# Optimization experiments

Hardware: AMD Instinct MI355X
Metric: run time of the kernel (lower is better)

The kernel has to match this reference:

```python
import jax, jax.numpy as jnp
import numpy as np

BS, T, N, M, P = 1024, 128, 128, 256, 256


def _lstm_cell(xin, h, c, Wih, Whh, bih, bhh):
    # PyTorch LSTMCell: gates ordered i, f, g, o
    z = xin @ Wih.T + bih + h @ Whh.T + bhh
    i, f, g, o = jnp.split(z, 4, axis=1)
    i = jax.nn.sigmoid(i); f = jax.nn.sigmoid(f)
    g = jnp.tanh(g); o = jax.nn.sigmoid(o)
    c2 = f * c + i * g
    return o * jnp.tanh(c2), c2


def setup_inputs() -> dict:
    key = jax.random.key(0)
    ks = jax.random.split(key, 24)
    s = 0.05
    return {
        "x": jax.random.normal(ks[0], (BS, T, N), jnp.float32),
        "y_known": jax.random.normal(ks[1], (BS, T, 1), jnp.float32),
        "We": jax.random.normal(ks[2], (T, 2 * M), jnp.float32) * s,
        "Ue": jax.random.normal(ks[3], (T, T), jnp.float32) * s,
        "Ve": jax.random.normal(ks[4], (1, T), jnp.float32) * s,
        "Wih_e": jax.random.normal(ks[5], (4 * M, N), jnp.float32) * s,
        "Whh_e": jax.random.normal(ks[6], (4 * M, M), jnp.float32) * s,
        "bih_e": jax.random.normal(ks[7], (4 * M,), jnp.float32) * s,
        "bhh_e": jax.random.normal(ks[8], (4 * M,), jnp.float32) * s,
        "Wd": jax.random.normal(ks[9], (M, 2 * P), jnp.float32) * s,
        "Ud": jax.random.normal(ks[10], (M, M), jnp.float32) * s,
        "Vd": jax.random.normal(ks[11], (1, M), jnp.float32) * s,
        "Wih_d": jax.random.normal(ks[12], (4 * P, 1), jnp.float32) * s,
        "Whh_d": jax.random.normal(ks[13], (4 * P, P), jnp.float32) * s,
        "bih_d": jax.random.normal(ks[14], (4 * P,), jnp.float32) * s,
        "bhh_d": jax.random.normal(ks[15], (4 * P,), jnp.float32) * s,
        "Wt": jax.random.normal(ks[16], (1, M + 1), jnp.float32) * s,
        "bt": jax.random.normal(ks[17], (1,), jnp.float32) * s,
        "W1": jax.random.normal(ks[18], (P, P + M), jnp.float32) * s,
        "b1": jax.random.normal(ks[19], (P,), jnp.float32) * s,
        "W2": jax.random.normal(ks[20], (1, P), jnp.float32) * s,
        "b2": jax.random.normal(ks[21], (1,), jnp.float32) * s,
    }


def reference(x, y_known, We, Ue, Ve, Wih_e, Whh_e, bih_e, bhh_e,
              Wd, Ud, Vd, Wih_d, Whh_d, bih_d, bhh_d,
              Wt, bt, W1, b1, W2, b2):
    bs, Tl, n = x.shape
    m = Whh_e.shape[1]
    p = Whh_d.shape[1]

    # ---- encoder (input attention) ----
    # U_e(x.permute(0,2,1)): loop-invariant, hoisted. (bs, n, T)
    Ux = jnp.einsum('btn,st->bns', x, Ue)

    def enc_step(carry, _):
        h, s = carry
        hs = jnp.concatenate([h, s], axis=1)            # (bs, 2m)
        ohs = hs @ We.T                                  # (bs, T)
        tanh_sum = jnp.tanh(ohs[:, None, :] + Ux)        # (bs, n, T)
        e = jnp.einsum('bnt,t->bn', tanh_sum, Ve[0])     # (bs, n)
        alpha = jax.nn.softmax(e, axis=1)
        xt = alpha * e                                   # faithful quirk: alpha * e_t
        h2, s2 = _lstm_cell(xt, h, s, Wih_e, Whh_e, bih_e, bhh_e)
        return (h2, s2), h2

    z = jnp.zeros((bs, m), x.dtype)
    _, h_all = jax.lax.scan(enc_step, (z, z), None, length=Tl)
    x1 = jnp.transpose(h_all, (1, 2, 0))                 # (bs, m, T)

    # ---- decoder (temporal attention) ----
    Udx = jnp.einsum('bmt,km->btk', x1, Ud)              # (bs, T, m)

    def dec_step(carry, yt):
        d, s, _ = carry
        ds = jnp.concatenate([d, s], axis=1)             # (bs, 2p)
        ods = ds @ Wd.T                                   # (bs, m)
        tanh_sum = jnp.tanh(ods[:, None, :] + Udx)        # (bs, T, m)
        l = jnp.einsum('btm,m->bt', tanh_sum, Vd[0])      # (bs, T)
        beta = jax.nn.softmax(l, axis=1)
        c = jnp.einsum('bt,bmt->bm', beta, x1)            # (bs, m)
        y_tilde = jnp.concatenate([yt, c], axis=1) @ Wt.T + bt  # (bs, 1)
        d2, s2 = _lstm_cell(y_tilde, d, s, Wih_d, Whh_d, bih_d, bhh_d)
        return (d2, s2, c), None

    zp = jnp.zeros((bs, p), x.dtype)
    zc = jnp.zeros((bs, m), x.dtype)
    (d, _, c), _ = jax.lax.scan(dec_step, (zp, zp, zc),
                                jnp.transpose(y_known, (1, 0, 2)))
    out1 = jnp.concatenate([d, c], axis=1) @ W1.T + b1
    return out1 @ W2.T + b2
```

## Files before the change

kernel.cpp:

```cpp
#include <hip/hip_runtime.h>


typedef unsigned int   uint;
typedef unsigned short ushort;
typedef _Float16 h2v __attribute__((ext_vector_type(2)));

#define O_WEH     0u
#define O_WENCH   32768u
#define O_WDH     229376u
#define O_WHHDH   294912u
#define O_UDT     425984u
#define O_UET     491520u
#define O_W1T     507904u
#define O_BENC    638976u
#define O_BDEC    640000u
#define W_FLOATS  641024u
#define O_X1H     641024u
#define O_BUF     17418240u
#define WS_FLOATS 34195456u

#define C2E 2.8853900817779268f
#define L2E 1.4426950408889634f

#define FMA4(acc, s, w) \
  acc.x = fmaf((s), (w).x, acc.x); \
  acc.y = fmaf((s), (w).y, acc.y); \
  acc.z = fmaf((s), (w).z, acc.z); \
  acc.w = fmaf((s), (w).w, acc.w);

union H2U { uint u; h2v h; _Float16 hs[2]; };

__device__ __forceinline__ float fdot2u(uint w, uint s, float acc) {
  H2U a; a.u = w; H2U b; b.u = s;
  return __builtin_amdgcn_fdot2(a.h, b.h, acc, false);
}
__device__ __forceinline__ uint pk2(float lo, float hi) {
  H2U v; v.hs[0] = (_Float16)lo; v.hs[1] = (_Float16)hi; return v.u;
}
__device__ __forceinline__ float h2lo(uint u) { H2U v; v.u = u; return (float)v.hs[0]; }
__device__ __forceinline__ float h2hi(uint u) { H2U v; v.u = u; return (float)v.hs[1]; }

__device__ __forceinline__ float fsig(float x) {
  return __builtin_amdgcn_rcpf(1.f + __builtin_amdgcn_exp2f(-L2E * x));
}
__device__ __forceinline__ float fth(float x) {
  float r = __builtin_amdgcn_rcpf(1.f + __builtin_amdgcn_exp2f(C2E * x));
  return fmaf(-2.f, r, 1.f);
}

#define DOT8(w, s0, s1) { \
  a0 = fdot2u(w.x, s0, a0); a1 = fdot2u(w.y, s0, a1); \
  a2 = fdot2u(w.z, s0, a2); a3 = fdot2u(w.w, s0, a3); \
  b0 = fdot2u(w.x, s1, b0); b1 = fdot2u(w.y, s1, b1); \
  b2 = fdot2u(w.z, s1, b2); b3 = fdot2u(w.w, s1, b3); }

#define ATT_TERM(vv, uu, oo) \
  ((vv) * __builtin_amdgcn_rcpf(1.f + __builtin_amdgcn_exp2f(fmaf(C2E, (uu), (oo)))))

__global__ __launch_bounds__(256) void prep_k(
    const float* __restrict__ We,    const float* __restrict__ Wih_e,
    const float* __restrict__ Whh_e, const float* __restrict__ Wd,
    const float* __restrict__ Whh_d, const float* __restrict__ W1,
    const float* __restrict__ Ud,    const float* __restrict__ Ue,
    const float* __restrict__ bih_e, const float* __restrict__ bhh_e,
    const float* __restrict__ bih_d, const float* __restrict__ bhh_d,
    float* __restrict__ ws)
{
  uint* wsu = (uint*)ws;
  unsigned idx = blockIdx.x * 256u + threadIdx.x;
  if (idx >= W_FLOATS) return;
  if (idx < 32768u) {
    unsigned kp = idx >> 7, j = idx & 127u;
    wsu[O_WEH + idx] = pk2(We[j * 512u + 2u*kp], We[j * 512u + 2u*kp + 1u]);
  } else if (idx < 229376u) {
    unsigned rel = idx - 32768u;
    unsigned kp = rel >> 10, j = rel & 1023u;
    float v0, v1;
    if (kp < 64u) { v0 = Wih_e[j * 128u + 2u*kp];          v1 = Wih_e[j * 128u + 2u*kp + 1u]; }
    else { unsigned k0 = 2u*(kp - 64u); v0 = Whh_e[j * 256u + k0]; v1 = Whh_e[j * 256u + k0 + 1u]; }
    wsu[O_WENCH + rel] = pk2(v0, v1);
  } else if (idx < 294912u) {
    unsigned rel = idx - 229376u;
    unsigned kp = rel >> 8, kk = rel & 255u;
    wsu[O_WDH + rel] = pk2(Wd[kk * 512u + 2u*kp], Wd[kk * 512u + 2u*kp + 1u]);
  } else if (idx < 425984u) {
    unsigned rel = idx - 294912u;
    unsigned kp = rel >> 10, j = rel & 1023u;
    wsu[O_WHHDH + rel] = pk2(Whh_d[j * 256u + 2u*kp], Whh_d[j * 256u + 2u*kp + 1u]);
  } else if (idx < 491520u) {
    unsigned rel = idx - 425984u;
    unsigned m = rel >> 8, k = rel & 255u;
    ws[O_UDT + rel] = Ud[k * 256u + m];
  } else if (idx < 507904u) {
    unsigned rel = idx - 491520u;
    unsigned t = rel >> 7, s = rel & 127u;
    ws[O_UET + rel] = Ue[s * 128u + t];
  } else if (idx < 638976u) {
    unsigned rel = idx - 507904u;
    unsigned k = rel >> 8, q = rel & 255u;
    ws[O_W1T + rel] = W1[q * 512u + k];
  } else if (idx < 640000u) {
    unsigned rel = idx - 638976u;
    ws[O_BENC + rel] = bih_e[rel] + bhh_e[rel];
  } else {
    unsigned rel = idx - 640000u;
    ws[O_BDEC + rel] = bih_d[rel] + bhh_d[rel];
  }
}

__global__ __launch_bounds__(256) void ux_k(
    const float* __restrict__ x, const float* __restrict__ UeT,
    uint* __restrict__ UxU)
{
  __shared__ float xs[128][32];
  const int b  = blockIdx.x >> 2;
  const int i0 = (blockIdx.x & 3) * 32;
  const int tid = threadIdx.x;
  for (int idx = tid; idx < 4096; idx += 256) {
    int t = idx >> 5, il = idx & 31;
    xs[t][il] = x[(size_t)b * 16384 + t * 128 + i0 + il];
  }
  __syncthreads();
  const int sl = tid & 31;
  const int ig = tid >> 5;
  const float4* UeT4 = (const float4*)UeT;
  float4 acc[4];
  #pragma unroll
  for (int ii = 0; ii < 4; ++ii) acc[ii] = make_float4(0.f, 0.f, 0.f, 0.f);
  for (int t = 0; t < 128; ++t) {
    float4 w = UeT4[t * 32 + sl];
    #pragma unroll
    for (int ii = 0; ii < 4; ++ii) {
      float a = xs[t][ig + 8 * ii];
      FMA4(acc[ii], a, w);
    }
  }
  uint2* U2 = (uint2*)UxU;
  #pragma unroll
  for (int ii = 0; ii < 4; ++ii) {
    int i_loc = i0 + ig + 8 * ii;
    uint2 pk;
    pk.x = pk2(acc[ii].x, acc[ii].y);
    pk.y = pk2(acc[ii].z, acc[ii].w);
    U2[((size_t)b * 128 + i_loc) * 32 + sl] = pk;
  }
}

__global__ __launch_bounds__(256) void udx_k(
    const uint* __restrict__ x1hU, const float* __restrict__ UdT,
    uint* __restrict__ UdxU)
{
  __shared__ float xs[32][256];
  const int b  = blockIdx.x >> 2;
  const int t0 = (blockIdx.x & 3) * 32;
  const int tid = threadIdx.x;
  const uint4* x14 = (const uint4*)x1hU + (size_t)b * 4096;
  for (int it = 0; it < 4; ++it) {
    int f = tid + it * 256;
    int tl = f >> 5, mq = f & 31;
    uint4 u = x14[(size_t)(t0 + tl) * 32 + mq];
    float* d = &xs[tl][mq * 8];
    d[0] = h2lo(u.x); d[1] = h2hi(u.x); d[2] = h2lo(u.y); d[3] = h2hi(u.y);
    d[4] = h2lo(u.z); d[5] = h2hi(u.z); d[6] = h2lo(u.w); d[7] = h2hi(u.w);
  }
  __syncthreads();
  const int kl = tid & 63;
  const int tg = tid >> 6;
  const float4* UdT4 = (const float4*)UdT;
  float4 acc[8];
  #pragma unroll
  for (int tt = 0; tt < 8; ++tt) acc[tt] = make_float4(0.f, 0.f, 0.f, 0.f);
  for (int m = 0; m < 256; ++m) {
    float4 w = UdT4[m * 64 + kl];
    #pragma unroll
    for (int tt = 0; tt < 8; ++tt) {
      float a = xs[tg + 4 * tt][m];
      FMA4(acc[tt], a, w);
    }
  }
  uint2* U2 = (uint2*)UdxU;
  #pragma unroll
  for (int tt = 0; tt < 8; ++tt) {
    uint2 pk;
    pk.x = pk2(acc[tt].x, acc[tt].y);
    pk.y = pk2(acc[tt].z, acc[tt].w);
    U2[((size_t)b * 128 + t0 + tg + 4 * tt) * 64 + kl] = pk;
  }
}

__global__ __launch_bounds__(512, 4) void encoder_k(
    const uint* __restrict__ WeH, const uint* __restrict__ WencH,
    const float* __restrict__ benc, const float* __restrict__ Ve,
    const uint* __restrict__ UxH, uint* __restrict__ x1hU)
{
  __shared__ uint stH[2][256];
  __shared__ uint xtH[2][64];
  __shared__ __align__(16) float part[4096];
  __shared__ float ohs2[2][128];
  __shared__ float bencS[1024];
  __shared__ float VeS[128];
  __shared__ float red[8];

  const int tid = threadIdx.x;
  const int b0 = blockIdx.x * 2;

  ((uint*)stH)[tid] = 0u;
  for (int i = tid; i < 1024; i += 512) bencS[i] = benc[i];
  if (tid < 128) VeS[tid] = Ve[tid];
  __syncthreads();

  float SVe = 0.f;
  for (int s = 0; s < 128; ++s) SVe += Ve[s];

  const uint4* WeH4   = (const uint4*)WeH;
  const uint4* WencH4 = (const uint4*)WencH;
  float4* part4 = (float4*)part;

  const int rB = tid >> 8, iB = (tid >> 1) & 127, sh = tid & 1;
  const uint4* ux4 = (const uint4*)UxH + ((size_t)(b0 + rB) * 128 + iB) * 16 + sh * 8;

  float c_reg = 0.f;

  for (int step = 0; step < 128; ++step) {
    {
      const int j4 = tid & 31, ks = tid >> 5;
      float a0=0,a1=0,a2=0,a3=0,b0=0,b1=0,b2=0,b3=0;
      const int kb = ks * 16;
      __builtin_amdgcn_s_setprio(1);
      #pragma unroll 4
      for (int kp = kb; kp < kb + 16; ++kp) {
        uint4 w = WeH4[kp * 32 + j4];
        uint s0 = stH[0][kp], s1 = stH[1][kp];
        DOT8(w, s0, s1);
      }
      __builtin_amdgcn_s_setprio(0);
      part4[(ks * 2 + 0) * 32 + j4] = make_float4(a0, a1, a2, a3);
      part4[(ks * 2 + 1) * 32 + j4] = make_float4(b0, b1, b2, b3);
    }
    __syncthreads();
    if (tid < 256) {
      const int r = tid >> 7, j = tid & 127;
      float acc = 0.f;
      #pragma unroll
      for (int ks = 0; ks < 16; ++ks) acc += part[(ks * 2 + r) * 128 + j];
      ohs2[r][j] = acc * C2E;
    }
    __syncthreads();
    float e_val;
    {
      float a0 = 0.f, a1 = 0.f, a2 = 0.f, a3 = 0.f;
      const float* oh = ohs2[rB];
      #pragma unroll 4
      for (int so = 0; so < 8; ++so) {
        uint4 u = ux4[so];
        const int s = sh * 64 + so * 8;
        a0 += ATT_TERM(VeS[s+0], h2lo(u.x), oh[s+0]);
        a1 += ATT_TERM(VeS[s+1], h2hi(u.x), oh[s+1]);
        a2 += ATT_TERM(VeS[s+2], h2lo(u.y), oh[s+2]);
        a3 += ATT_TERM(VeS[s+3], h2hi(u.y), oh[s+3]);
        a0 += ATT_TERM(VeS[s+4], h2lo(u.z), oh[s+4]);
        a1 += ATT_TERM(VeS[s+5], h2hi(u.z), oh[s+5]);
        a2 += ATT_TERM(VeS[s+6], h2lo(u.w), oh[s+6]);
        a3 += ATT_TERM(VeS[s+7], h2hi(u.w), oh[s+7]);
      }
      float r4 = (a0 + a1) + (a2 + a3);
      r4 += __shfl_xor(r4, 1);
      e_val = fmaf(-2.f, r4, SVe);
    }
    {
      float p  = __builtin_amdgcn_exp2f(L2E * e_val);
      float ps = (sh == 0) ? p : 0.f;
      #pragma unroll
      for (int o = 1; o < 64; o <<= 1) ps += __shfl_xor(ps, o);
      if ((tid & 63) == 0) red[tid >> 6] = ps;
      __syncthreads();
      const int base = (tid >> 6) & 4;
      float sm = (red[base+0] + red[base+1]) + (red[base+2] + red[base+3]);
      float xt = p * __builtin_amdgcn_rcpf(sm) * e_val;
      float xn = __shfl_down(xt, 2);
      if ((tid & 3) == 0) xtH[rB][iB >> 1] = pk2(xt, xn);
    }
    __syncthreads();
    {
      const int j4 = tid & 255, ks = tid >> 8;
      float a0=0,a1=0,a2=0,a3=0,b0=0,b1=0,b2=0,b3=0;
      __builtin_amdgcn_s_setprio(1);
      if (ks == 0) {
        #pragma unroll 2
        for (int kp = 0; kp < 64; ++kp) {
          uint4 w = WencH4[kp * 256 + j4];
          uint s0 = xtH[0][kp], s1 = xtH[1][kp];
          DOT8(w, s0, s1);
        }
        #pragma unroll 2
        for (int kp = 64; kp < 96; ++kp) {
          uint4 w = WencH4[kp * 256 + j4];
          uint s0 = stH[0][kp - 64], s1 = stH[1][kp - 64];
          DOT8(w, s0, s1);
        }
      } else {
        #pragma unroll 2
        for (int kp = 96; kp < 192; ++kp) {
          uint4 w = WencH4[kp * 256 + j4];
          uint s0 = stH[0][kp - 64], s1 = stH[1][kp - 64];
          DOT8(w, s0, s1);
        }
      }
      __builtin_amdgcn_s_setprio(0);
      part4[(ks * 2 + 0) * 256 + j4] = make_float4(a0, a1, a2, a3);
      part4[(ks * 2 + 1) * 256 + j4] = make_float4(b0, b1, b2, b3);
    }
    __syncthreads();
    {
      const int r = tid >> 8, j = tid & 255;
      float z0 = bencS[j]       + part[r * 1024 + j]       + part[(2 + r) * 1024 + j];
      float z1 = bencS[256 + j] + part[r * 1024 + 256 + j] + part[(2 + r) * 1024 + 256 + j];
      float z2 = bencS[512 + j] + part[r * 1024 + 512 + j] + part[(2 + r) * 1024 + 512 + j];
      float z3 = bencS[768 + j] + part[r * 1024 + 768 + j] + part[(2 + r) * 1024 + 768 + j];
      float gi = fsig(z0), gf = fsig(z1), gg = fth(z2), go = fsig(z3);
      float c2 = fmaf(gf, c_reg, gi * gg);
      c_reg = c2;
      float h2 = go * fth(c2);
      float hn = __shfl_down(h2, 1);
      float cn = __shfl_down(c2, 1);
      if (!(j & 1)) {
        uint hp = pk2(h2, hn), cp = pk2(c2, cn);
        stH[r][j >> 1] = hp;
        stH[r][128 + (j >> 1)] = cp;
        x1hU[((size_t)(b0 + r) * 128 + step) * 128 + (j >> 1)] = hp;
      }
    }
    __syncthreads();
  }
}

__global__ __launch_bounds__(512, 4) void decoder_k(
    const uint* __restrict__ WdH, const uint* __restrict__ WhhdH,
    const float* __restrict__ W1T, const float* __restrict__ bdec,
    const float* __restrict__ Vd,  const float* __restrict__ WihD,
    const float* __restrict__ Wt,  const float* __restrict__ btp,
    const float* __restrict__ b1,  const float* __restrict__ W2,
    const float* __restrict__ b2p, const float* __restrict__ yk,
    const uint* __restrict__ UdxH, const uint* __restrict__ x1hU,
    float* __restrict__ out)
{
  __shared__ uint stH[2][256];
  __shared__ __align__(16) float part[4096];
  __shared__ float ods2[2][256];
  __shared__ float cT[2][256];
  __shared__ float betaS[2][128];
  __shared__ float wihdS[1024];
  __shared__ float bdecS[1024];
  __shared__ float VdS[256];
  __shared__ float yts[2];
  __shared__ float red[8];

  const int tid = threadIdx.x;
  const int b0 = blockIdx.x * 2;

  ((uint*)stH)[tid] = 0u;
  for (int i = tid; i < 1024; i += 512) { wihdS[i] = WihD[i]; bdecS[i] = bdec[i]; }
  if (tid < 256) VdS[tid] = Vd[tid];
  __syncthreads();

  float SVd = 0.f;
  for (int k = 0; k < 256; ++k) SVd += Vd[k];

  const float bt0 = btp[0], Wt0 = Wt[0];
  const uint4*  WdH4   = (const uint4*)WdH;
  const uint4*  WhhdH4 = (const uint4*)WhhdH;
  const float4* W1T4   = (const float4*)W1T;
  float4* part4 = (float4*)part;

  const int rB = tid >> 8, tB = (tid >> 1) & 127, kh = tid & 1;
  const uint4* ud4 = (const uint4*)UdxH + ((size_t)(b0 + rB) * 128 + tB) * 32 + kh * 16;
  const int m8 = tid & 31, rb2 = (tid >> 5) & 1, ts = tid >> 6;
  const uint4* x14 = (const uint4*)x1hU + (size_t)(b0 + rb2) * 4096 + m8;

  float c_reg = 0.f;

  for (int step = 0; step < 128; ++step) {
    float ykv = 0.f;
    if ((tid & 255) == 0) ykv = yk[(size_t)(b0 + (tid >> 8)) * 128 + step];
    {
      const int j4 = tid & 63, ks = tid >> 6;
      float a0=0,a1=0,a2=0,a3=0,b0=0,b1=0,b2=0,b3=0;
      const int kb = ks * 32;
      __builtin_amdgcn_s_setprio(1);
      #pragma unroll 4
      for (int kp = kb; kp < kb + 32; ++kp) {
        uint4 w = WdH4[kp * 64 + j4];
        uint s0 = stH[0][kp], s1 = stH[1][kp];
        DOT8(w, s0, s1);
      }
      __builtin_amdgcn_s_setprio(0);
      part4[(ks * 2 + 0) * 64 + j4] = make_float4(a0, a1, a2, a3);
      part4[(ks * 2 + 1) * 64 + j4] = make_float4(b0, b1, b2, b3);
    }
    __syncthreads();
    {
      const int r = tid >> 8, kk = tid & 255;
      float acc = 0.f;
      #pragma unroll
      for (int ks = 0; ks < 8; ++ks) acc += part[(ks * 2 + r) * 256 + kk];
      ods2[r][kk] = acc * C2E;
    }
    __syncthreads();
    float l_val;
    {
      float a0 = 0.f, a1 = 0.f, a2 = 0.f, a3 = 0.f;
      const float* od = ods2[rB];
      #pragma unroll 4
      for (int ko = 0; ko < 16; ++ko) {
        uint4 u = ud4[ko];
        const int k = kh * 128 + ko * 8;
        a0 += ATT_TERM(VdS[k+0], h2lo(u.x), od[k+0]);
        a1 += ATT_TERM(VdS[k+1], h2hi(u.x), od[k+1]);
        a2 += ATT_TERM(VdS[k+2], h2lo(u.y), od[k+2]);
        a3 += ATT_TERM(VdS[k+3], h2hi(u.y), od[k+3]);
        a0 += ATT_TERM(VdS[k+4], h2lo(u.z), od[k+4]);
        a1 += ATT_TERM(VdS[k+5], h2hi(u.z), od[k+5]);
        a2 += ATT_TERM(VdS[k+6], h2lo(u.w), od[k+6]);
        a3 += ATT_TERM(VdS[k+7], h2hi(u.w), od[k+7]);
      }
      float r4 = (a0 + a1) + (a2 + a3);
      r4 += __shfl_xor(r4, 1);
      l_val = fmaf(-2.f, r4, SVd);
    }
    {
      float p  = __builtin_amdgcn_exp2f(L2E * l_val);
      float ps = (kh == 0) ? p : 0.f;
      #pragma unroll
      for (int o = 1; o < 64; o <<= 1) ps += __shfl_xor(ps, o);
      if ((tid & 63) == 0) red[tid >> 6] = ps;
      __syncthreads();
      const int base = (tid >> 6) & 4;
      float sm = (red[base+0] + red[base+1]) + (red[base+2] + red[base+3]);
      if (kh == 0) betaS[rB][tB] = p * __builtin_amdgcn_rcpf(sm);
    }
    __syncthreads();
    {
      float c0=0,c1=0,c2=0,c3=0,c4=0,c5=0,c6=0,c7=0;
      const float* bS = betaS[rb2];
      #pragma unroll 4
      for (int tt = 0; tt < 16; ++tt) {
        const int t = ts * 16 + tt;
        float bv = bS[t];
        uint4 u = x14[(size_t)t * 32];
        c0 = fmaf(bv, h2lo(u.x), c0); c1 = fmaf(bv, h2hi(u.x), c1);
        c2 = fmaf(bv, h2lo(u.y), c2); c3 = fmaf(bv, h2hi(u.y), c3);
        c4 = fmaf(bv, h2lo(u.z), c4); c5 = fmaf(bv, h2hi(u.z), c5);
        c6 = fmaf(bv, h2lo(u.w), c6); c7 = fmaf(bv, h2hi(u.w), c7);
      }
      part4[(ts * 2 + rb2) * 64 + m8 * 2]     = make_float4(c0, c1, c2, c3);
      part4[(ts * 2 + rb2) * 64 + m8 * 2 + 1] = make_float4(c4, c5, c6, c7);
    }
    __syncthreads();
    {
      const int r = tid >> 8, m = tid & 255;
      float v = 0.f;
      #pragma unroll
      for (int t8 = 0; t8 < 8; ++t8) v += part[(t8 * 2 + r) * 256 + m];
      cT[r][m] = v;
      float pv = v * Wt[1 + m];
      #pragma unroll
      for (int o = 1; o < 64; o <<= 1) pv += __shfl_xor(pv, o);
      if ((tid & 63) == 0) red[tid >> 6] = pv;
      __syncthreads();
      if ((tid & 255) == 0) {
        const int base = r * 4;
        float s = (red[base] + red[base+1]) + (red[base+2] + red[base+3]);
        yts[r] = s + ykv * Wt0 + bt0;
      }
    }
    {
      const int j4 = tid & 255, ks = tid >> 8;
      float a0=0,a1=0,a2=0,a3=0,b0=0,b1=0,b2=0,b3=0;
      const int kb = ks * 64;
      __builtin_amdgcn_s_setprio(1);
      #pragma unroll 2
      for (int kp = kb; kp < kb + 64; ++kp) {
        uint4 w = WhhdH4[kp * 256 + j4];
        uint s0 = stH[0][kp], s1 = stH[1][kp];
        DOT8(w, s0, s1);
      }
      __builtin_amdgcn_s_setprio(0);
      part4[(ks * 2 + 0) * 256 + j4] = make_float4(a0, a1, a2, a3);
      part4[(ks * 2 + 1) * 256 + j4] = make_float4(b0, b1, b2, b3);
    }
    __syncthreads();
    {
      const int r = tid >> 8, j = tid & 255;
      float yt = yts[r];
      float z0 = fmaf(yt, wihdS[j],       bdecS[j])       + part[r * 1024 + j]       + part[(2 + r) * 1024 + j];
      float z1 = fmaf(yt, wihdS[256 + j], bdecS[256 + j]) + part[r * 1024 + 256 + j] + part[(2 + r) * 1024 + 256 + j];
      float z2 = fmaf(yt, wihdS[512 + j], bdecS[512 + j]) + part[r * 1024 + 512 + j] + part[(2 + r) * 1024 + 512 + j];
      float z3 = fmaf(yt, wihdS[768 + j], bdecS[768 + j]) + part[r * 1024 + 768 + j] + part[(2 + r) * 1024 + 768 + j];
      float gi = fsig(z0), gf = fsig(z1), gg = fth(z2), go = fsig(z3);
      float c2 = fmaf(gf, c_reg, gi * gg);
      c_reg = c2;
      float d2 = go * fth(c2);
      float dn = __shfl_down(d2, 1);
      float cn = __shfl_down(c2, 1);
      if (!(j & 1)) {
        stH[r][j >> 1] = pk2(d2, dn);
        stH[r][128 + (j >> 1)] = pk2(c2, cn);
      }
    }
    __syncthreads();
  }
  {
    const int l = tid & 63, ks = tid >> 6;
    float a0=0,a1=0,a2=0,a3=0,b0=0,b1=0,b2=0,b3=0;
    const int kb = ks * 64;
    if (ks < 4) {
      for (int k = kb; k < kb + 64; ++k) {
        float4 w = W1T4[k * 64 + l];
        uint u0 = stH[0][k >> 1], u1 = stH[1][k >> 1];
        float d0 = (k & 1) ? h2hi(u0) : h2lo(u0);
        float d1 = (k & 1) ? h2hi(u1) : h2lo(u1);
        a0=fmaf(d0,w.x,a0); a1=fmaf(d0,w.y,a1); a2=fmaf(d0,w.z,a2); a3=fmaf(d0,w.w,a3);
        b0=fmaf(d1,w.x,b0); b1=fmaf(d1,w.y,b1); b2=fmaf(d1,w.z,b2); b3=fmaf(d1,w.w,b3);
      }
    } else {
      for (int k = kb; k < kb + 64; ++k) {
        float4 w = W1T4[k * 64 + l];
        float c0 = cT[0][k - 256], c1 = cT[1][k - 256];
        a0=fmaf(c0,w.x,a0); a1=fmaf(c0,w.y,a1); a2=fmaf(c0,w.z,a2); a3=fmaf(c0,w.w,a3);
        b0=fmaf(c1,w.x,b0); b1=fmaf(c1,w.y,b1); b2=fmaf(c1,w.z,b2); b3=fmaf(c1,w.w,b3);
      }
    }
    part4[(ks * 2 + 0) * 64 + l] = make_float4(a0, a1, a2, a3);
    part4[(ks * 2 + 1) * 64 + l] = make_float4(b0, b1, b2, b3);
  }
  __syncthreads();
  {
    const int r = tid >> 8, q = tid & 255;
    float o1 = b1[q];
    #pragma unroll
    for (int ks = 0; ks < 8; ++ks) o1 += part[(ks * 2 + r) * 256 + q];
    float pv = o1 * W2[q];
    #pragma unroll
    for (int o = 1; o < 64; o <<= 1) pv += __shfl_xor(pv, o);
    if ((tid & 63) == 0) red[tid >> 6] = pv;
    __syncthreads();
    if ((tid & 255) == 0) {
      const int base = r * 4;
      float s = (red[base] + red[base+1]) + (red[base+2] + red[base+3]);
      out[b0 + r] = s + b2p[0];
    }
  }
}

extern "C" void kernel_launch(void* const* d_in, const int* in_sizes, int n_in,
                              void* d_out, int out_size, void* d_ws, size_t ws_size,
                              hipStream_t stream)
{
  const float* x       = (const float*)d_in[0];
  const float* y_known = (const float*)d_in[1];
  const float* We      = (const float*)d_in[2];
  const float* Ue      = (const float*)d_in[3];
  const float* Ve      = (const float*)d_in[4];
  const float* Wih_e   = (const float*)d_in[5];
  const float* Whh_e   = (const float*)d_in[6];
  const float* bih_e   = (const float*)d_in[7];
  const float* bhh_e   = (const float*)d_in[8];
  const float* Wd      = (const float*)d_in[9];
  const float* Ud      = (const float*)d_in[10];
  const float* Vd      = (const float*)d_in[11];
  const float* Wih_d   = (const float*)d_in[12];
  const float* Whh_d   = (const float*)d_in[13];
  const float* bih_d   = (const float*)d_in[14];
  const float* bhh_d   = (const float*)d_in[15];
  const float* Wt      = (const float*)d_in[16];
  const float* bt      = (const float*)d_in[17];
  const float* W1      = (const float*)d_in[18];
  const float* b1      = (const float*)d_in[19];
  const float* W2      = (const float*)d_in[20];
  const float* b2      = (const float*)d_in[21];

  float* ws  = (float*)d_ws;
  float* out = (float*)d_out;
  if (ws_size < (size_t)WS_FLOATS * 4u) return;

  uint* wsu  = (uint*)ws;
  uint* x1hU = (uint*)(ws + O_X1H);
  uint* bufU = (uint*)(ws + O_BUF);

  prep_k<<<(W_FLOATS + 255) / 256, 256, 0, stream>>>(
      We, Wih_e, Whh_e, Wd, Whh_d, W1, Ud, Ue,
      bih_e, bhh_e, bih_d, bhh_d, ws);

  ux_k<<<4096, 256, 0, stream>>>(x, ws + O_UET, bufU);
  encoder_k<<<512, 512, 0, stream>>>(wsu + O_WEH, wsu + O_WENCH,
                                     ws + O_BENC, Ve, bufU, x1hU);
  udx_k<<<4096, 256, 0, stream>>>(x1hU, ws + O_UDT, bufU);
  decoder_k<<<512, 512, 0, stream>>>(wsu + O_WDH, wsu + O_WHHDH,
                                     ws + O_W1T, ws + O_BDEC, Vd, Wih_d,
                                     Wt, bt, b1, W2, b2, y_known,
                                     bufU, x1hU, out);
}
```

Measured before the change: 6.981 ms.

## Fuse encoder, Ud projection and decoder into one kernel with per-batch arena

Merges the encoder, the Udx projection and the decoder into a single kernel. Each block now computes Udx for its own two batch rows between the encoder and decoder phases instead of relying on a separate 4096-block GEMM launch. Workspace is reorganised into a per-batch arena that holds x1 and the Ux/Udx buffer contiguously, and shared memory is aliased across phases. The intent is to drop two kernel launches and improve locality. The cost is that the Udx GEMM now runs inside only 512 blocks, serialised with the recurrences.

```diff
diff --git a/kernel.cpp b/kernel.cpp
--- a/kernel.cpp
+++ b/kernel.cpp
@@ -15,8 +15,7 @@
 #define O_BENC    638976u
 #define O_BDEC    640000u
 #define W_FLOATS  641024u
-#define O_X1H     641024u
-#define O_BUF     17418240u
+#define O_AR      641024u
 #define WS_FLOATS 34195456u
 
 #define C2E 2.8853900817779268f
@@ -110,7 +109,7 @@
 
 __global__ __launch_bounds__(256) void ux_k(
     const float* __restrict__ x, const float* __restrict__ UeT,
-    uint* __restrict__ UxU)
+    uint* __restrict__ AR)
 {
   __shared__ float xs[128][32];
   const int b  = blockIdx.x >> 2;
@@ -135,230 +134,231 @@
       FMA4(acc[ii], a, w);
     }
   }
-  uint2* U2 = (uint2*)UxU;
+  uint2* U2 = (uint2*)(AR + (size_t)b * 32768 + 16384);
   #pragma unroll
   for (int ii = 0; ii < 4; ++ii) {
     int i_loc = i0 + ig + 8 * ii;
     uint2 pk;
     pk.x = pk2(acc[ii].x, acc[ii].y);
     pk.y = pk2(acc[ii].z, acc[ii].w);
-    U2[((size_t)b * 128 + i_loc) * 32 + sl] = pk;
-  }
-}
-
-__global__ __launch_bounds__(256) void udx_k(
-    const uint* __restrict__ x1hU, const float* __restrict__ UdT,
-    uint* __restrict__ UdxU)
-{
-  __shared__ float xs[32][256];
-  const int b  = blockIdx.x >> 2;
-  const int t0 = (blockIdx.x & 3) * 32;
-  const int tid = threadIdx.x;
-  const uint4* x14 = (const uint4*)x1hU + (size_t)b * 4096;
-  for (int it = 0; it < 4; ++it) {
-    int f = tid + it * 256;
-    int tl = f >> 5, mq = f & 31;
-    uint4 u = x14[(size_t)(t0 + tl) * 32 + mq];
-    float* d = &xs[tl][mq * 8];
-    d[0] = h2lo(u.x); d[1] = h2hi(u.x); d[2] = h2lo(u.y); d[3] = h2hi(u.y);
-    d[4] = h2lo(u.z); d[5] = h2hi(u.z); d[6] = h2lo(u.w); d[7] = h2hi(u.w);
-  }
-  __syncthreads();
-  const int kl = tid & 63;
-  const int tg = tid >> 6;
-  const float4* UdT4 = (const float4*)UdT;
-  float4 acc[8];
-  #pragma unroll
-  for (int tt = 0; tt < 8; ++tt) acc[tt] = make_float4(0.f, 0.f, 0.f, 0.f);
-  for (int m = 0; m < 256; ++m) {
-    float4 w = UdT4[m * 64 + kl];
-    #pragma unroll
-    for (int tt = 0; tt < 8; ++tt) {
-      float a = xs[tg + 4 * tt][m];
-      FMA4(acc[tt], a, w);
-    }
-  }
-  uint2* U2 = (uint2*)UdxU;
-  #pragma unroll
-  for (int tt = 0; tt < 8; ++tt) {
-    uint2 pk;
-    pk.x = pk2(acc[tt].x, acc[tt].y);
-    pk.y = pk2(acc[tt].z, acc[tt].w);
-    U2[((size_t)b * 128 + t0 + tg + 4 * tt) * 64 + kl] = pk;
-  }
-}
-
-__global__ __launch_bounds__(512, 4) void encoder_k(
-    const uint* __restrict__ WeH, const uint* __restrict__ WencH,
+    U2[i_loc * 32 + sl] = pk;
+  }
+}
+
+__global__ __launch_bounds__(512, 4) void fused_k(
+    const uint* __restrict__ WeH,  const uint* __restrict__ WencH,
     const float* __restrict__ benc, const float* __restrict__ Ve,
-    const uint* __restrict__ UxH, uint* __restrict__ x1hU)
-{
-  __shared__ uint stH[2][256];
-  __shared__ uint xtH[2][64];
-  __shared__ __align__(16) float part[4096];
-  __shared__ float ohs2[2][128];
-  __shared__ float bencS[1024];
-  __shared__ float VeS[128];
-  __shared__ float red[8];
-
-  const int tid = threadIdx.x;
-  const int b0 = blockIdx.x * 2;
-
-  ((uint*)stH)[tid] = 0u;
-  for (int i = tid; i < 1024; i += 512) bencS[i] = benc[i];
-  if (tid < 128) VeS[tid] = Ve[tid];
-  __syncthreads();
-
-  float SVe = 0.f;
-  for (int s = 0; s < 128; ++s) SVe += Ve[s];
-
-  const uint4* WeH4   = (const uint4*)WeH;
-  const uint4* WencH4 = (const uint4*)WencH;
-  float4* part4 = (float4*)part;
-
-  const int rB = tid >> 8, iB = (tid >> 1) & 127, sh = tid & 1;
-  const uint4* ux4 = (const uint4*)UxH + ((size_t)(b0 + rB) * 128 + iB) * 16 + sh * 8;
-
-  float c_reg = 0.f;
-
-  for (int step = 0; step < 128; ++step) {
-    {
-      const int j4 = tid & 31, ks = tid >> 5;
-      float a0=0,a1=0,a2=0,a3=0,b0=0,b1=0,b2=0,b3=0;
-      const int kb = ks * 16;
-      __builtin_amdgcn_s_setprio(1);
-      #pragma unroll 4
-      for (int kp = kb; kp < kb + 16; ++kp) {
-        uint4 w = WeH4[kp * 32 + j4];
-        uint s0 = stH[0][kp], s1 = stH[1][kp];
-        DOT8(w, s0, s1);
-      }
-      __builtin_amdgcn_s_setprio(0);
-      part4[(ks * 2 + 0) * 32 + j4] = make_float4(a0, a1, a2, a3);
-      part4[(ks * 2 + 1) * 32 + j4] = make_float4(b0, b1, b2, b3);
-    }
-    __syncthreads();
-    if (tid < 256) {
-      const int r = tid >> 7, j = tid & 127;
-      float acc = 0.f;
-      #pragma unroll
-      for (int ks = 0; ks < 16; ++ks) acc += part[(ks * 2 + r) * 128 + j];
-      ohs2[r][j] = acc * C2E;
-    }
-    __syncthreads();
-    float e_val;
-    {
-      float a0 = 0.f, a1 = 0.f, a2 = 0.f, a3 = 0.f;
-      const float* oh = ohs2[rB];
-      #pragma unroll 4
-      for (int so = 0; so < 8; ++so) {
-        uint4 u = ux4[so];
-        const int s = sh * 64 + so * 8;
-        a0 += ATT_TERM(VeS[s+0], h2lo(u.x), oh[s+0]);
-        a1 += ATT_TERM(VeS[s+1], h2hi(u.x), oh[s+1]);
-        a2 += ATT_TERM(VeS[s+2], h2lo(u.y), oh[s+2]);
-        a3 += ATT_TERM(VeS[s+3], h2hi(u.y), oh[s+3]);
-        a0 += ATT_TERM(VeS[s+4], h2lo(u.z), oh[s+4]);
-        a1 += ATT_TERM(VeS[s+5], h2hi(u.z), oh[s+5]);
-        a2 += ATT_TERM(VeS[s+6], h2lo(u.w), oh[s+6]);
-        a3 += ATT_TERM(VeS[s+7], h2hi(u.w), oh[s+7]);
-      }
-      float r4 = (a0 + a1) + (a2 + a3);
-      r4 += __shfl_xor(r4, 1);
-      e_val = fmaf(-2.f, r4, SVe);
-    }
-    {
-      float p  = __builtin_amdgcn_exp2f(L2E * e_val);
-      float ps = (sh == 0) ? p : 0.f;
-      #pragma unroll
-      for (int o = 1; o < 64; o <<= 1) ps += __shfl_xor(ps, o);
-      if ((tid & 63) == 0) red[tid >> 6] = ps;
-      __syncthreads();
-      const int base = (tid >> 6) & 4;
-      float sm = (red[base+0] + red[base+1]) + (red[base+2] + red[base+3]);
-      float xt = p * __builtin_amdgcn_rcpf(sm) * e_val;
-      float xn = __shfl_down(xt, 2);
-      if ((tid & 3) == 0) xtH[rB][iB >> 1] = pk2(xt, xn);
-    }
-    __syncthreads();
-    {
-      const int j4 = tid & 255, ks = tid >> 8;
-      float a0=0,a1=0,a2=0,a3=0,b0=0,b1=0,b2=0,b3=0;
-      __builtin_amdgcn_s_setprio(1);
-      if (ks == 0) {
-        #pragma unroll 2
-        for (int kp = 0; kp < 64; ++kp) {
-          uint4 w = WencH4[kp * 256 + j4];
-          uint s0 = xtH[0][kp], s1 = xtH[1][kp];
-          DOT8(w, s0, s1);
-        }
-        #pragma unroll 2
-        for (int kp = 64; kp < 96; ++kp) {
-          uint4 w = WencH4[kp * 256 + j4];
-          uint s0 = stH[0][kp - 64], s1 = stH[1][kp - 64];
-          DOT8(w, s0, s1);
-        }
-      } else {
-        #pragma unroll 2
-        for (int kp = 96; kp < 192; ++kp) {
-          uint4 w = WencH4[kp * 256 + j4];
-          uint s0 = stH[0][kp - 64], s1 = stH[1][kp - 64];
-          DOT8(w, s0, s1);
-        }
-      }
-      __builtin_amdgcn_s_setprio(0);
-      part4[(ks * 2 + 0) * 256 + j4] = make_float4(a0, a1, a2, a3);
-      part4[(ks * 2 + 1) * 256 + j4] = make_float4(b0, b1, b2, b3);
-    }
-    __syncthreads();
-    {
-      const int r = tid >> 8, j = tid & 255;
-      float z0 = bencS[j]       + part[r * 1024 + j]       + part[(2 + r) * 1024 + j];
-      float z1 = bencS[256 + j] + part[r * 1024 + 256 + j] + part[(2 + r) * 1024 + 256 + j];
-      float z2 = bencS[512 + j] + part[r * 1024 + 512 + j] + part[(2 + r) * 1024 + 512 + j];
-      float z3 = bencS[768 + j] + part[r * 1024 + 768 + j] + part[(2 + r) * 1024 + 768 + j];
-      float gi = fsig(z0), gf = fsig(z1), gg = fth(z2), go = fsig(z3);
-      float c2 = fmaf(gf, c_reg, gi * gg);
-      c_reg = c2;
-      float h2 = go * fth(c2);
-      float hn = __shfl_down(h2, 1);
-      float cn = __shfl_down(c2, 1);
-      if (!(j & 1)) {
-        uint hp = pk2(h2, hn), cp = pk2(c2, cn);
-        stH[r][j >> 1] = hp;
-        stH[r][128 + (j >> 1)] = cp;
-        x1hU[((size_t)(b0 + r) * 128 + step) * 128 + (j >> 1)] = hp;
-      }
-    }
-    __syncthreads();
-  }
-}
-
-__global__ __launch_bounds__(512, 4) void decoder_k(
-    const uint* __restrict__ WdH, const uint* __restrict__ WhhdH,
+    const float* __restrict__ UdT,
+    const uint* __restrict__ WdH,  const uint* __restrict__ WhhdH,
     const float* __restrict__ W1T, const float* __restrict__ bdec,
     const float* __restrict__ Vd,  const float* __restrict__ WihD,
     const float* __restrict__ Wt,  const float* __restrict__ btp,
     const float* __restrict__ b1,  const float* __restrict__ W2,
     const float* __restrict__ b2p, const float* __restrict__ yk,
-    const uint* __restrict__ UdxH, const uint* __restrict__ x1hU,
-    float* __restrict__ out)
+    uint* __restrict__ AR, float* __restrict__ out)
 {
-  __shared__ uint stH[2][256];
-  __shared__ __align__(16) float part[4096];
-  __shared__ float ods2[2][256];
-  __shared__ float cT[2][256];
-  __shared__ float betaS[2][128];
-  __shared__ float wihdS[1024];
-  __shared__ float bdecS[1024];
-  __shared__ float VdS[256];
-  __shared__ float yts[2];
-  __shared__ float red[8];
+  __shared__ __align__(16) float smemF[12288];
+  float*  part  = smemF;
+  float4* part4 = (float4*)smemF;
+  uint*  stE   = (uint*)(smemF + 4096);
+  uint*  xtH   = (uint*)(smemF + 4608);
+  float* ohs2  = smemF + 4736;
+  float* bencS = smemF + 4992;
+  float* VeS   = smemF + 6016;
+  float* redE  = smemF + 6144;
+  float* xs    = smemF + 4096;
+  uint*  stD   = (uint*)(smemF + 4096);
+  float* ods2  = smemF + 4608;
+  float* cT    = smemF + 5120;
+  float* betaS = smemF + 5632;
+  float* wihdS = smemF + 5888;
+  float* bdecS = smemF + 6912;
+  float* VdS   = smemF + 7936;
+  float* yts   = smemF + 8192;
+  float* redD  = smemF + 8194;
 
   const int tid = threadIdx.x;
   const int b0 = blockIdx.x * 2;
-
-  ((uint*)stH)[tid] = 0u;
+  uint* ar0 = AR + (size_t)b0 * 32768;
+  uint* ar1 = ar0 + 32768;
+
+  stE[tid] = 0u;
+  for (int i = tid; i < 1024; i += 512) bencS[i] = benc[i];
+  if (tid < 128) VeS[tid] = Ve[tid];
+  __syncthreads();
+
+  float SVe = 0.f;
+  for (int s = 0; s < 128; ++s) SVe += Ve[s];
+
+  const uint4* WeH4   = (const uint4*)WeH;
+  const uint4* WencH4 = (const uint4*)WencH;
+
+  {
+    const int rB = tid >> 8, iB = (tid >> 1) & 127, sh = tid & 1;
+    const uint4* ux4 = (const uint4*)((rB ? ar1 : ar0) + 16384) + iB * 16 + sh * 8;
+    float c_reg = 0.f;
+
+    for (int step = 0; step < 128; ++step) {
+      {
+        const int j4 = tid & 31, ks = tid >> 5;
+        float a0=0,a1=0,a2=0,a3=0,b0_=0,b1_=0,b2_=0,b3_=0;
+        const int kb = ks * 16;
+        __builtin_amdgcn_s_setprio(1);
+        #pragma unroll 4
+        for (int kp = kb; kp < kb + 16; ++kp) {
+          uint4 w = WeH4[kp * 32 + j4];
+          uint s0 = stE[kp], s1 = stE[256 + kp];
+          float b0=b0_, b1=b1_, b2=b2_, b3=b3_;
+          DOT8(w, s0, s1);
+          b0_=b0; b1_=b1; b2_=b2; b3_=b3;
+        }
+        __builtin_amdgcn_s_setprio(0);
+        part4[(ks * 2 + 0) * 32 + j4] = make_float4(a0, a1, a2, a3);
+        part4[(ks * 2 + 1) * 32 + j4] = make_float4(b0_, b1_, b2_, b3_);
+      }
+      __syncthreads();
+      if (tid < 256) {
+        const int r = tid >> 7, j = tid & 127;
+        float acc = 0.f;
+        #pragma unroll
+        for (int ks = 0; ks < 16; ++ks) acc += part[(ks * 2 + r) * 128 + j];
+        ohs2[r * 128 + j] = acc * C2E;
+      }
+      __syncthreads();
+      float e_val;
+      {
+        float a0 = 0.f, a1 = 0.f, a2 = 0.f, a3 = 0.f;
+        const float* oh = ohs2 + rB * 128;
+        #pragma unroll 4
+        for (int so = 0; so < 8; ++so) {
+          uint4 u = ux4[so];
+          const int s = sh * 64 + so * 8;
+          a0 += ATT_TERM(VeS[s+0], h2lo(u.x), oh[s+0]);
+          a1 += ATT_TERM(VeS[s+1], h2hi(u.x), oh[s+1]);
+          a2 += ATT_TERM(VeS[s+2], h2lo(u.y), oh[s+2]);
+          a3 += ATT_TERM(VeS[s+3], h2hi(u.y), oh[s+3]);
+          a0 += ATT_TERM(VeS[s+4], h2lo(u.z), oh[s+4]);
+          a1 += ATT_TERM(VeS[s+5], h2hi(u.z), oh[s+5]);
+          a2 += ATT_TERM(VeS[s+6], h2lo(u.w), oh[s+6]);
+          a3 += ATT_TERM(VeS[s+7], h2hi(u.w), oh[s+7]);
+        }
+        float r4 = (a0 + a1) + (a2 + a3);
+        r4 += __shfl_xor(r4, 1);
+        e_val = fmaf(-2.f, r4, SVe);
+      }
+      {
+        float p  = __builtin_amdgcn_exp2f(L2E * e_val);
+        float ps = (sh == 0) ? p : 0.f;
+        #pragma unroll
+        for (int o = 1; o < 64; o <<= 1) ps += __shfl_xor(ps, o);
+        if ((tid & 63) == 0) redE[tid >> 6] = ps;
+        __syncthreads();
+        const int base = (tid >> 6) & 4;
+        float sm = (redE[base+0] + redE[base+1]) + (redE[base+2] + redE[base+3]);
+        float xt = p * __builtin_amdgcn_rcpf(sm) * e_val;
+        float xn = __shfl_down(xt, 2);
+        if ((tid & 3) == 0) xtH[rB * 64 + (iB >> 1)] = pk2(xt, xn);
+      }
+      __syncthreads();
+      {
+        const int j4 = tid & 255, ks = tid >> 8;
+        float a0=0,a1=0,a2=0,a3=0,b0_=0,b1_=0,b2_=0,b3_=0;
+        __builtin_amdgcn_s_setprio(1);
+        if (ks == 0) {
+          #pragma unroll 2
+          for (int kp = 0; kp < 64; ++kp) {
+            uint4 w = WencH4[kp * 256 + j4];
+            uint s0 = xtH[kp], s1 = xtH[64 + kp];
+            float b0=b0_, b1=b1_, b2=b2_, b3=b3_;
+            DOT8(w, s0, s1);
+            b0_=b0; b1_=b1; b2_=b2; b3_=b3;
+          }
+          #pragma unroll 2
+          for (int kp = 64; kp < 96; ++kp) {
+            uint4 w = WencH4[kp * 256 + j4];
+            uint s0 = stE[kp - 64], s1 = stE[256 + kp - 64];
+            float b0=b0_, b1=b1_, b2=b2_, b3=b3_;
+            DOT8(w, s0, s1);
+            b0_=b0; b1_=b1; b2_=b2; b3_=b3;
+          }
+        } else {
+          #pragma unroll 2
+          for (int kp = 96; kp < 192; ++kp) {
+            uint4 w = WencH4[kp * 256 + j4];
+            uint s0 = stE[kp - 64], s1 = stE[256 + kp - 64];
+            float b0=b0_, b1=b1_, b2=b2_, b3=b3_;
+            DOT8(w, s0, s1);
+            b0_=b0; b1_=b1; b2_=b2; b3_=b3;
+          }
+        }
+        __builtin_amdgcn_s_setprio(0);
+        part4[(ks * 2 + 0) * 256 + j4] = make_float4(a0, a1, a2, a3);
+        part4[(ks * 2 + 1) * 256 + j4] = make_float4(b0_, b1_, b2_, b3_);
+      }
+      __syncthreads();
+      {
+        const int r = tid >> 8, j = tid & 255;
+        float z0 = bencS[j]       + part[r * 1024 + j]       + part[(2 + r) * 1024 + j];
+        float z1 = bencS[256 + j] + part[r * 1024 + 256 + j] + part[(2 + r) * 1024 + 256 + j];
+        float z2 = bencS[512 + j] + part[r * 1024 + 512 + j] + part[(2 + r) * 1024 + 512 + j];
+        float z3 = bencS[768 + j] + part[r * 1024 + 768 + j] + part[(2 + r) * 1024 + 768 + j];
+        float gi = fsig(z0), gf = fsig(z1), gg = fth(z2), go = fsig(z3);
+        float c2 = fmaf(gf, c_reg, gi * gg);
+        c_reg = c2;
+        float h2 = go * fth(c2);
+        float hn = __shfl_down(h2, 1);
+        float cn = __shfl_down(c2, 1);
+        if (!(j & 1)) {
+          uint hp = pk2(h2, hn), cp = pk2(c2, cn);
+          stE[r * 256 + (j >> 1)] = hp;
+          stE[r * 256 + 128 + (j >> 1)] = cp;
+          (r ? ar1 : ar0)[step * 128 + (j >> 1)] = hp;
+        }
+      }
+      __syncthreads();
+    }
+  }
+
+  {
+    const float4* UdT4 = (const float4*)UdT;
+    for (int sub = 0; sub < 8; ++sub) {
+      const int r = sub >> 2, t0 = (sub & 3) * 32;
+      const uint4* x14s = (const uint4*)(r ? ar1 : ar0);
+      #pragma unroll
+      for (int it = 0; it < 2; ++it) {
+        int f = tid + it * 512;
+        int tl = f >> 5, mq = f & 31;
+        uint4 u = x14s[(size_t)(t0 + tl) * 32 + mq];
+        float* d = &xs[tl * 256 + mq * 8];
+        d[0]=h2lo(u.x); d[1]=h2hi(u.x); d[2]=h2lo(u.y); d[3]=h2hi(u.y);
+        d[4]=h2lo(u.z); d[5]=h2hi(u.z); d[6]=h2lo(u.w); d[7]=h2hi(u.w);
+      }
+      __syncthreads();
+      const int kl = tid & 63, tg = tid >> 6;
+      float4 acc[4];
+      #pragma unroll
+      for (int tt = 0; tt < 4; ++tt) acc[tt] = make_float4(0.f, 0.f, 0.f, 0.f);
+      for (int m = 0; m < 256; ++m) {
+        float4 w = UdT4[m * 64 + kl];
+        #pragma unroll
+        for (int tt = 0; tt < 4; ++tt) {
+          float a = xs[(tg + 8 * tt) * 256 + m];
+          FMA4(acc[tt], a, w);
+        }
+      }
+      uint2* U2 = (uint2*)((r ? ar1 : ar0) + 16384);
+      #pragma unroll
+      for (int tt = 0; tt < 4; ++tt) {
+        uint2 pk;
+        pk.x = pk2(acc[tt].x, acc[tt].y);
+        pk.y = pk2(acc[tt].z, acc[tt].w);
+        U2[(size_t)(t0 + tg + 8 * tt) * 64 + kl] = pk;
+      }
+      __syncthreads();
+    }
+  }
+
+  stD[tid] = 0u;
   for (int i = tid; i < 1024; i += 512) { wihdS[i] = WihD[i]; bdecS[i] = bdec[i]; }
   if (tid < 256) VdS[tid] = Vd[tid];
   __syncthreads();
@@ -370,12 +370,11 @@
   const uint4*  WdH4   = (const uint4*)WdH;
   const uint4*  WhhdH4 = (const uint4*)WhhdH;
   const float4* W1T4   = (const float4*)W1T;
-  float4* part4 = (float4*)part;
 
   const int rB = tid >> 8, tB = (tid >> 1) & 127, kh = tid & 1;
-  const uint4* ud4 = (const uint4*)UdxH + ((size_t)(b0 + rB) * 128 + tB) * 32 + kh * 16;
+  const uint4* ud4 = (const uint4*)((rB ? ar1 : ar0) + 16384) + tB * 32 + kh * 16;
   const int m8 = tid & 31, rb2 = (tid >> 5) & 1, ts = tid >> 6;
-  const uint4* x14 = (const uint4*)x1hU + (size_t)(b0 + rb2) * 4096 + m8;
+  const uint4* x14 = (const uint4*)(rb2 ? ar1 : ar0) + m8;
 
   float c_reg = 0.f;
 
@@ -384,18 +383,20 @@
     if ((tid & 255) == 0) ykv = yk[(size_t)(b0 + (tid >> 8)) * 128 + step];
     {
       const int j4 = tid & 63, ks = tid >> 6;
-      float a0=0,a1=0,a2=0,a3=0,b0=0,b1=0,b2=0,b3=0;
+      float a0=0,a1=0,a2=0,a3=0,b0_=0,b1_=0,b2_=0,b3_=0;
       const int kb = ks * 32;
       __builtin_amdgcn_s_setprio(1);
       #pragma unroll 4
       for (int kp = kb; kp < kb + 32; ++kp) {
         uint4 w = WdH4[kp * 64 + j4];
-        uint s0 = stH[0][kp], s1 = stH[1][kp];
+        uint s0 = stD[kp], s1 = stD[256 + kp];
+        float b0=b0_, b1=b1_, b2=b2_, b3=b3_;
         DOT8(w, s0, s1);
+        b0_=b0; b1_=b1; b2_=b2; b3_=b3;
       }
       __builtin_amdgcn_s_setprio(0);
       part4[(ks * 2 + 0) * 64 + j4] = make_float4(a0, a1, a2, a3);
-      part4[(ks * 2 + 1) * 64 + j4] = make_float4(b0, b1, b2, b3);
+      part4[(ks * 2 + 1) * 64 + j4] = make_float4(b0_, b1_, b2_, b3_);
     }
     __syncthreads();
     {
@@ -403,13 +404,13 @@
       float acc = 0.f;
       #pragma unroll
       for (int ks = 0; ks < 8; ++ks) acc += part[(ks * 2 + r) * 256 + kk];
-      ods2[r][kk] = acc * C2E;
+      ods2[r * 256 + kk] = acc * C2E;
     }
     __syncthreads();
     float l_val;
     {
       float a0 = 0.f, a1 = 0.f, a2 = 0.f, a3 = 0.f;
-      const float* od = ods2[rB];
+      const float* od = ods2 + rB * 256;
       #pragma unroll 4
       for (int ko = 0; ko < 16; ++ko) {
         uint4 u = ud4[ko];
@@ -432,16 +433,16 @@
       float ps = (kh == 0) ? p : 0.f;
       #pragma unroll
       for (int o = 1; o < 64; o <<= 1) ps += __shfl_xor(ps, o);
-      if ((tid & 63) == 0) red[tid >> 6] = ps;
+      if ((tid & 63) == 0) redD[tid >> 6] = ps;
       __syncthreads();
       const int base = (tid >> 6) & 4;
-      float sm = (red[base+0] + red[base+1]) + (red[base+2] + red[base+3]);
-      if (kh == 0) betaS[rB][tB] = p * __builtin_amdgcn_rcpf(sm);
+      float sm = (redD[base+0] + redD[base+1]) + (redD[base+2] + redD[base+3]);
+      if (kh == 0) betaS[rB * 128 + tB] = p * __builtin_amdgcn_rcpf(sm);
     }
     __syncthreads();
     {
       float c0=0,c1=0,c2=0,c3=0,c4=0,c5=0,c6=0,c7=0;
-      const float* bS = betaS[rb2];
+      const float* bS = betaS + rb2 * 128;
       #pragma unroll 4
       for (int tt = 0; tt < 16; ++tt) {
         const int t = ts * 16 + tt;
@@ -461,32 +462,34 @@
       float v = 0.f;
       #pragma unroll
       for (int t8 = 0; t8 < 8; ++t8) v += part[(t8 * 2 + r) * 256 + m];
-      cT[r][m] = v;
+      cT[r * 256 + m] = v;
       float pv = v * Wt[1 + m];
       #pragma unroll
       for (int o = 1; o < 64; o <<= 1) pv += __shfl_xor(pv, o);
-      if ((tid & 63) == 0) red[tid >> 6] = pv;
+      if ((tid & 63) == 0) redD[tid >> 6] = pv;
       __syncthreads();
       if ((tid & 255) == 0) {
         const int base = r * 4;
-        float s = (red[base] + red[base+1]) + (red[base+2] + red[base+3]);
+        float s = (redD[base] + redD[base+1]) + (redD[base+2] + redD[base+3]);
         yts[r] = s + ykv * Wt0 + bt0;
       }
     }
     {
       const int j4 = tid & 255, ks = tid >> 8;
-      float a0=0,a1=0,a2=0,a3=0,b0=0,b1=0,b2=0,b3=0;
+      float a0=0,a1=0,a2=0,a3=0,b0_=0,b1_=0,b2_=0,b3_=0;
       const int kb = ks * 64;
       __builtin_amdgcn_s_setprio(1);
       #pragma unroll 2
       for (int kp = kb; kp < kb + 64; ++kp) {
         uint4 w = WhhdH4[kp * 256 + j4];
-        uint s0 = stH[0][kp], s1 = stH[1][kp];
+        uint s0 = stD[kp], s1 = stD[256 + kp];
+        float b0=b0_, b1=b1_, b2=b2_, b3=b3_;
         DOT8(w, s0, s1);
+        b0_=b0; b1_=b1; b2_=b2; b3_=b3;
       }
       __builtin_amdgcn_s_setprio(0);
       part4[(ks * 2 + 0) * 256 + j4] = make_float4(a0, a1, a2, a3);
-      part4[(ks * 2 + 1) * 256 + j4] = make_float4(b0, b1, b2, b3);
+      part4[(ks * 2 + 1) * 256 + j4] = make_float4(b0_, b1_, b2_, b3_);
     }
     __syncthreads();
     {
@@ -503,35 +506,35 @@
       float dn = __shfl_down(d2, 1);
       float cn = __shfl_down(c2, 1);
       if (!(j & 1)) {
-        stH[r][j >> 1] = pk2(d2, dn);
-        stH[r][128 + (j >> 1)] = pk2(c2, cn);
+        stD[r * 256 + (j >> 1)] = pk2(d2, dn);
+        stD[r * 256 + 128 + (j >> 1)] = pk2(c2, cn);
       }
     }
     __syncthreads();
   }
   {
     const int l = tid & 63, ks = tid >> 6;
-    float a0=0,a1=0,a2=0,a3=0,b0=0,b1=0,b2=0,b3=0;
+    float a0=0,a1=0,a2=0,a3=0,b0_=0,b1_=0,b2_=0,b3_=0;
     const int kb = ks * 64;
     if (ks < 4) {
       for (int k = kb; k < kb + 64; ++k) {
         float4 w = W1T4[k * 64 + l];
-        uint u0 = stH[0][k >> 1], u1 = stH[1][k >> 1];
+        uint u0 = stD[k >> 1], u1 = stD[256 + (k >> 1)];
         float d0 = (k & 1) ? h2hi(u0) : h2lo(u0);
         float d1 = (k & 1) ? h2hi(u1) : h2lo(u1);
         a0=fmaf(d0,w.x,a0); a1=fmaf(d0,w.y,a1); a2=fmaf(d0,w.z,a2); a3=fmaf(d0,w.w,a3);
-        b0=fmaf(d1,w.x,b0); b1=fmaf(d1,w.y,b1); b2=fmaf(d1,w.z,b2); b3=fmaf(d1,w.w,b3);
+        b0_=fmaf(d1,w.x,b0_); b1_=fmaf(d1,w.y,b1_); b2_=fmaf(d1,w.z,b2_); b3_=fmaf(d1,w.w,b3_);
       }
     } else {
       for (int k = kb; k < kb + 64; ++k) {
         float4 w = W1T4[k * 64 + l];
-        float c0 = cT[0][k - 256], c1 = cT[1][k - 256];
+        float c0 = cT[k - 256], c1 = cT[256 + k - 256];
         a0=fmaf(c0,w.x,a0); a1=fmaf(c0,w.y,a1); a2=fmaf(c0,w.z,a2); a3=fmaf(c0,w.w,a3);
-        b0=fmaf(c1,w.x,b0); b1=fmaf(c1,w.y,b1); b2=fmaf(c1,w.z,b2); b3=fmaf(c1,w.w,b3);
+        b0_=fmaf(c1,w.x,b0_); b1_=fmaf(c1,w.y,b1_); b2_=fmaf(c1,w.z,b2_); b3_=fmaf(c1,w.w,b3_);
       }
     }
     part4[(ks * 2 + 0) * 64 + l] = make_float4(a0, a1, a2, a3);
-    part4[(ks * 2 + 1) * 64 + l] = make_float4(b0, b1, b2, b3);
+    part4[(ks * 2 + 1) * 64 + l] = make_float4(b0_, b1_, b2_, b3_);
   }
   __syncthreads();
   {
@@ -542,11 +545,11 @@
     float pv = o1 * W2[q];
     #pragma unroll
     for (int o = 1; o < 64; o <<= 1) pv += __shfl_xor(pv, o);
-    if ((tid & 63) == 0) red[tid >> 6] = pv;
+    if ((tid & 63) == 0) redD[tid >> 6] = pv;
     __syncthreads();
     if ((tid & 255) == 0) {
       const int base = r * 4;
-      float s = (red[base] + red[base+1]) + (red[base+2] + red[base+3]);
+      float s = (redD[base] + redD[base+1]) + (redD[base+2] + redD[base+3]);
       out[b0 + r] = s + b2p[0];
     }
   }
@@ -583,20 +586,18 @@
   float* out = (float*)d_out;
   if (ws_size < (size_t)WS_FLOATS * 4u) return;
 
-  uint* wsu  = (uint*)ws;
-  uint* x1hU = (uint*)(ws + O_X1H);
-  uint* bufU = (uint*)(ws + O_BUF);
+  uint* wsu = (uint*)ws;
+  uint* AR  = (uint*)(ws + O_AR);
 
   prep_k<<<(W_FLOATS + 255) / 256, 256, 0, stream>>>(
       We, Wih_e, Whh_e, Wd, Whh_d, W1, Ud, Ue,
       bih_e, bhh_e, bih_d, bhh_d, ws);
 
-  ux_k<<<4096, 256, 0, stream>>>(x, ws + O_UET, bufU);
-  encoder_k<<<512, 512, 0, stream>>>(wsu + O_WEH, wsu + O_WENCH,
-                                     ws + O_BENC, Ve, bufU, x1hU);
-  udx_k<<<4096, 256, 0, stream>>>(x1hU, ws + O_UDT, bufU);
-  decoder_k<<<512, 512, 0, stream>>>(wsu + O_WDH, wsu + O_WHHDH,
-                                     ws + O_W1T, ws + O_BDEC, Vd, Wih_d,
-                                     Wt, bt, b1, W2, b2, y_known,
-                                     bufU, x1hU, out);
-}
+  ux_k<<<4096, 256, 0, stream>>>(x, ws + O_UET, AR);
+  fused_k<<<512, 512, 0, stream>>>(wsu + O_WEH, wsu + O_WENCH,
+                                   ws + O_BENC, Ve, ws + O_UDT,
+                                   wsu + O_WDH, wsu + O_WHHDH,
+                                   ws + O_W1T, ws + O_BDEC, Vd, Wih_d,
+                                   Wt, bt, b1, W2, b2, y_known,
+                                   AR, out);
+}
```

New measurement: 6.893 ms (median of 2 runs). Within noise of the previous version (-1.3%).
